# Performance work log

Measured on AMD Instinct MI355X. Metric: run time of the kernel, lower is better.

Reference implementation:

```python
import jax, jax.numpy as jnp
import numpy as np

N = 150000   # nonempty octree nodes at this depth
CIN = 256
CB = 64      # bottleneck channels = out_channels / bottleneck
COUT = 256
G = 32       # group-norm groups
K = 27       # 3x3x3 neighborhood
EPS = 1e-5


def group_norm(x, gamma, beta, groups=G):
    # x: [N, C]; octree GN treats the N nodes as the spatial extent of one instance
    n, c = x.shape
    xg = x.reshape(n, groups, c // groups)
    mu = xg.mean(axis=(0, 2), keepdims=True)
    var = xg.var(axis=(0, 2), keepdims=True)
    xg = (xg - mu) * jax.lax.rsqrt(var + EPS)
    return xg.reshape(n, c) * gamma + beta


def setup_inputs() -> dict:
    key = jax.random.key(0)
    ks = jax.random.split(key, 5)
    return {
        "data": jax.random.normal(ks[0], (N, CIN), jnp.float32),
        "neigh": jax.random.randint(ks[1], (N, K), 0, N, jnp.int32),
        "w1a": jax.random.normal(ks[2], (CIN, CB), jnp.float32) * 0.05,
        "g1a": jnp.ones((CB,), jnp.float32),
        "b1a": jnp.zeros((CB,), jnp.float32),
        "w3": jax.random.normal(ks[3], (K, CB, CB), jnp.float32) * 0.05,
        "g3": jnp.ones((CB,), jnp.float32),
        "b3": jnp.zeros((CB,), jnp.float32),
        "w1b": jax.random.normal(ks[4], (CB, COUT), jnp.float32) * 0.05,
        "g1b": jnp.ones((COUT,), jnp.float32),
        "b1b": jnp.zeros((COUT,), jnp.float32),
    }


def reference(data, neigh, w1a, g1a, b1a, w3, g3, b3, w1b, g1b, b1b):
    # conv1x1a + GN + ReLU
    x = jax.nn.relu(group_norm(data @ w1a, g1a, b1a))
    # octree 3x3x3 sparse conv: gather 27 neighbors, GEMM against [27,CB,CB] kernel
    gathered = x[neigh]                      # [N, 27, CB]
    y = jnp.einsum('nkc,kcd->nd', gathered, w3)
    y = jax.nn.relu(group_norm(y, g3, b3))
    # conv1x1b + GN
    z = group_norm(y @ w1b, g1b, b1b)
    # residual add (in_channels == out_channels -> identity skip) + ReLU
    return jax.nn.relu(z + data)
```

## Files before the change

kernel.cpp:

```cpp
#include <hip/hip_runtime.h>
#include <math.h>

#define CIN 256
#define CB 64
#define COUT 256
#define KNB 27
#define EPS 1e-5f

typedef unsigned short u16;
typedef __attribute__((ext_vector_type(8))) short short8;
typedef __attribute__((ext_vector_type(4))) float f32x4;

typedef const __attribute__((address_space(1))) unsigned int* gas_u32p;
typedef __attribute__((address_space(3))) unsigned int* las_u32p;
#define GLL(g, p) __builtin_amdgcn_global_load_lds((gas_u32p)(const void*)(g), \
        (las_u32p)(void*)(p), 16, 0, 0)

__device__ inline short f2bf(float f) {
    union { float f; unsigned u; } v; v.f = f;
    unsigned r = v.u + 0x7fff + ((v.u >> 16) & 1);
    return (short)(r >> 16);
}
__device__ inline float bf2f(short s) {
    union { unsigned u; float f; } v; v.u = ((unsigned)(u16)s) << 16;
    return v.f;
}
__device__ inline short8 pack8(float4 x0, float4 x1) {
    short8 r;
    r[0] = f2bf(x0.x); r[1] = f2bf(x0.y); r[2] = f2bf(x0.z); r[3] = f2bf(x0.w);
    r[4] = f2bf(x1.x); r[5] = f2bf(x1.y); r[6] = f2bf(x1.z); r[7] = f2bf(x1.w);
    return r;
}

__global__ void k_prep(const float* __restrict__ w1a, const float* __restrict__ w3,
                       const float* __restrict__ w1b, u16* __restrict__ w1at,
                       u16* __restrict__ w3img, u16* __restrict__ w1bt)
{
    int i = blockIdx.x * 256 + threadIdx.x;
    if (i < 16384) {
        int k = i >> 6, d = i & 63;
        w1at[d * 256 + k] = (u16)f2bf(w1a[i]);
    } else if (i < 126976) {
        int j = i - 16384;
        int k = j >> 12, c = (j >> 6) & 63, d = j & 63;
        w3img[(size_t)k * 4096 + d * 64 + (c ^ ((d & 7) << 3))] = (u16)f2bf(w3[j]);
    } else if (i < 143360) {
        int j = i - 126976;
        int c = j >> 8, d = j & 255;
        w1bt[d * 64 + c] = (u16)f2bf(w1b[j]);
    }
}

__global__ __launch_bounds__(256) void k_gemm1(const float* __restrict__ data,
        const u16* __restrict__ w1at, u16* __restrict__ t1,
        float* __restrict__ stats, int n)
{
    __shared__ float s_sum[32], s_sq[32];
    const int tid = threadIdx.x;
    if (tid < 32) { s_sum[tid] = 0.f; s_sq[tid] = 0.f; }
    __syncthreads();
    const int l = tid & 63, wv = tid >> 6;
    const int ll = l & 15, lh = l >> 4;
    const int rowbase = blockIdx.x * 256 + wv * 64;

    f32x4 acc[4][4] = {};
#pragma unroll
    for (int kc = 0; kc < 8; ++kc) {
        short8 b[4];
#pragma unroll
        for (int f = 0; f < 4; ++f)
            b[f] = *(const short8*)(w1at + (size_t)(f * 16 + ll) * 256 + kc * 32 + lh * 8);
#pragma unroll
        for (int rt = 0; rt < 4; ++rt) {
            int row = rowbase + rt * 16 + ll;
            int rowc = (row < n) ? row : 0;
            const float* ar = data + (size_t)rowc * CIN + kc * 32 + lh * 8;
            short8 a = pack8(*(const float4*)ar, *(const float4*)(ar + 4));
#pragma unroll
            for (int f = 0; f < 4; ++f)
                acc[rt][f] = __builtin_amdgcn_mfma_f32_16x16x32_bf16(a, b[f], acc[rt][f], 0, 0, 0);
        }
    }
    float gs[4] = {0.f, 0.f, 0.f, 0.f}, gq[4] = {0.f, 0.f, 0.f, 0.f};
#pragma unroll
    for (int rt = 0; rt < 4; ++rt) {
#pragma unroll
        for (int f = 0; f < 4; ++f) {
#pragma unroll
            for (int r = 0; r < 4; ++r) {
                int rr = rowbase + rt * 16 + lh * 4 + r;
                if (rr < n) {
                    float v = acc[rt][f][r];
                    t1[(size_t)rr * CB + f * 16 + ll] = (u16)f2bf(v);
                    gs[f] += v; gq[f] += v * v;
                }
            }
        }
    }
#pragma unroll
    for (int f = 0; f < 4; ++f) {
        float s = gs[f], q = gq[f];
        s += __shfl_xor(s, 1); s += __shfl_xor(s, 16); s += __shfl_xor(s, 32);
        q += __shfl_xor(q, 1); q += __shfl_xor(q, 16); q += __shfl_xor(q, 32);
        if ((l & 0x31) == 0) {
            atomicAdd(&s_sum[f * 8 + (ll >> 1)], s);
            atomicAdd(&s_sq [f * 8 + (ll >> 1)], q);
        }
    }
    __syncthreads();
    if (tid < 32) {
        atomicAdd(&stats[tid], s_sum[tid]);
        atomicAdd(&stats[32 + tid], s_sq[tid]);
    }
}

__global__ void k_apply64(u16* __restrict__ buf, const float* __restrict__ st,
        const float* __restrict__ gamma, const float* __restrict__ beta, int n)
{
    const float cnt = (float)n * 2.0f;
    const int total = n * 8;
    for (int i = blockIdx.x * blockDim.x + threadIdx.x; i < total;
         i += gridDim.x * blockDim.x) {
        int c0 = (i & 7) * 8;
        short8 v = ((short8*)buf)[i];
#pragma unroll
        for (int j = 0; j < 8; ++j) {
            int c = c0 + j, g = c >> 1;
            float mu = st[g] / cnt;
            float var = st[32 + g] / cnt - mu * mu;
            float inv = rsqrtf(var + EPS);
            float x = bf2f(v[j]);
            x = fmaxf((x - mu) * inv * gamma[c] + beta[c], 0.f);
            v[j] = f2bf(x);
        }
        ((short8*)buf)[i] = v;
    }
}

__global__ __launch_bounds__(256) void k_conv(const u16* __restrict__ xb,
        const int* __restrict__ neigh, const u16* __restrict__ w3img,
        u16* __restrict__ y, float* __restrict__ stats, int n)
{
    __shared__ u16 s_w3[2][4096];
    __shared__ float s_sum[32], s_sq[32];
    const int tid = threadIdx.x;
    if (tid < 32) { s_sum[tid] = 0.f; s_sq[tid] = 0.f; }
    const int row0 = blockIdx.x * 128;
    const int l = tid & 63, wv = tid >> 6;
    const int ll = l & 15, lh = l >> 4;
    const int r0 = row0 + wv * 32 + ll;
    const int r1 = r0 + 16;
    const int r0c = (r0 < n) ? r0 : 0;
    const int r1c = (r1 < n) ? r1 : 0;
    const int* __restrict__ nrow0 = neigh + (size_t)r0c * KNB;
    const int* __restrict__ nrow1 = neigh + (size_t)r1c * KNB;

    u16* ld0 = &s_w3[0][0] + wv * 1024 + l * 8;
    u16* ld1 = &s_w3[1][0] + wv * 1024 + l * 8;
    const u16* gw = w3img + wv * 1024 + l * 8;

    GLL(gw, ld0);
    GLL(gw + 512, ld0 + 512);
    int ia = nrow0[0], ib = nrow1[0];
    {
        const u16* xa = xb + (size_t)ia * CB + lh * 8;
        const u16* xc = xb + (size_t)ib * CB + lh * 8;
        ia = nrow0[1]; ib = nrow1[1];
        __builtin_amdgcn_sched_barrier(0);
    }
    short8 a0c, a1c, a2c, a3c;
    {
        const u16* xa = xb + (size_t)nrow0[0] * CB + lh * 8;
        const u16* xc = xb + (size_t)nrow1[0] * CB + lh * 8;
        a0c = *(const short8*)xa; a1c = *(const short8*)(xa + 32);
        a2c = *(const short8*)xc; a3c = *(const short8*)(xc + 32);
    }
    __syncthreads();

    f32x4 acc[2][4] = {};
    for (int k = 0; k < KNB; ++k) {
        const int cur = k & 1;
        short8 a0n, a1n, a2n, a3n;
        if (k + 1 < KNB) {
            const u16* gsrc = w3img + (size_t)(k + 1) * 4096 + wv * 1024 + l * 8;
            u16* ldst = cur ? ld0 : ld1;
            GLL(gsrc, ldst);
            GLL(gsrc + 512, ldst + 512);
            int i2 = nrow0[k + 1], i3 = nrow1[k + 1];
            const u16* xa = xb + (size_t)i2 * CB + lh * 8;
            const u16* xc = xb + (size_t)i3 * CB + lh * 8;
            a0n = *(const short8*)xa; a1n = *(const short8*)(xa + 32);
            a2n = *(const short8*)xc; a3n = *(const short8*)(xc + 32);
        }
        __builtin_amdgcn_sched_barrier(0);
#pragma unroll
        for (int f = 0; f < 4; ++f) {
            int d = f * 16 + ll;
            int swz = (d & 7) << 4;
            short8 b0 = *(const short8*)((const char*)&s_w3[cur][0] + d * 128 + ((lh * 16) ^ swz));
            short8 b1 = *(const short8*)((const char*)&s_w3[cur][0] + d * 128 + ((64 + lh * 16) ^ swz));
            acc[0][f] = __builtin_amdgcn_mfma_f32_16x16x32_bf16(a0c, b0, acc[0][f], 0, 0, 0);
            acc[0][f] = __builtin_amdgcn_mfma_f32_16x16x32_bf16(a1c, b1, acc[0][f], 0, 0, 0);
            acc[1][f] = __builtin_amdgcn_mfma_f32_16x16x32_bf16(a2c, b0, acc[1][f], 0, 0, 0);
            acc[1][f] = __builtin_amdgcn_mfma_f32_16x16x32_bf16(a3c, b1, acc[1][f], 0, 0, 0);
        }
        if (k + 1 < KNB) { a0c = a0n; a1c = a1n; a2c = a2n; a3c = a3n; }
        __syncthreads();
    }
    float gs[4] = {0.f, 0.f, 0.f, 0.f}, gq[4] = {0.f, 0.f, 0.f, 0.f};
#pragma unroll
    for (int rt = 0; rt < 2; ++rt) {
#pragma unroll
        for (int f = 0; f < 4; ++f) {
#pragma unroll
            for (int r = 0; r < 4; ++r) {
                int rr = row0 + wv * 32 + rt * 16 + lh * 4 + r;
                if (rr < n) {
                    float v = acc[rt][f][r];
                    y[(size_t)rr * CB + f * 16 + ll] = (u16)f2bf(v);
                    gs[f] += v; gq[f] += v * v;
                }
            }
        }
    }
#pragma unroll
    for (int f = 0; f < 4; ++f) {
        float s = gs[f], q = gq[f];
        s += __shfl_xor(s, 1); s += __shfl_xor(s, 16); s += __shfl_xor(s, 32);
        q += __shfl_xor(q, 1); q += __shfl_xor(q, 16); q += __shfl_xor(q, 32);
        if ((l & 0x31) == 0) {
            atomicAdd(&s_sum[f * 8 + (ll >> 1)], s);
            atomicAdd(&s_sq [f * 8 + (ll >> 1)], q);
        }
    }
    __syncthreads();
    if (tid < 32) {
        atomicAdd(&stats[64 + tid], s_sum[tid]);
        atomicAdd(&stats[96 + tid], s_sq[tid]);
    }
}

__global__ __launch_bounds__(256) void k_gemm2(const u16* __restrict__ y2,
        const u16* __restrict__ w1bt, float* __restrict__ z, u16* __restrict__ zb,
        float* __restrict__ stats, const float* __restrict__ g3,
        const float* __restrict__ b3, int n)
{
    __shared__ float s_sum[8], s_sq[8];
    const int tid = threadIdx.x;
    if (tid < 8) { s_sum[tid] = 0.f; s_sq[tid] = 0.f; }
    __syncthreads();
    const int l = tid & 63, wv = tid >> 6;
    const int ll = l & 15, lh = l >> 4;
    const int rowbase = blockIdx.x * 256 + wv * 64;
    const int cb = blockIdx.y;

    const float* st2 = stats + 64;
    const float cnt2 = (float)n * 2.0f;
    float sc[16], sh[16];
#pragma unroll
    for (int j = 0; j < 16; ++j) {
        int c = (j < 8) ? (lh * 8 + j) : (32 + lh * 8 + (j - 8));
        int g = c >> 1;
        float mu = st2[g] / cnt2;
        float var = st2[32 + g] / cnt2 - mu * mu;
        float inv = rsqrtf(var + EPS);
        float gm = g3[c];
        sc[j] = inv * gm;
        sh[j] = b3[c] - mu * inv * gm;
    }

    short8 b0[4], b1[4];
#pragma unroll
    for (int f = 0; f < 4; ++f) {
        const u16* br = w1bt + (size_t)(cb * 64 + f * 16 + ll) * CB + lh * 8;
        b0[f] = *(const short8*)(br);
        b1[f] = *(const short8*)(br + 32);
    }
    f32x4 acc[4][4] = {};
#pragma unroll
    for (int rt = 0; rt < 4; ++rt) {
        int row = rowbase + rt * 16 + ll;
        int rowc = (row < n) ? row : 0;
        const u16* ar = y2 + (size_t)rowc * CB + lh * 8;
        short8 r0 = *(const short8*)(ar);
        short8 r1 = *(const short8*)(ar + 32);
        short8 a0, a1;
#pragma unroll
        for (int j = 0; j < 8; ++j) {
            a0[j] = f2bf(fmaxf(bf2f(r0[j]) * sc[j] + sh[j], 0.f));
            a1[j] = f2bf(fmaxf(bf2f(r1[j]) * sc[8 + j] + sh[8 + j], 0.f));
        }
#pragma unroll
        for (int f = 0; f < 4; ++f) {
            acc[rt][f] = __builtin_amdgcn_mfma_f32_16x16x32_bf16(a0, b0[f], acc[rt][f], 0, 0, 0);
            acc[rt][f] = __builtin_amdgcn_mfma_f32_16x16x32_bf16(a1, b1[f], acc[rt][f], 0, 0, 0);
        }
    }
    float gs[4] = {0.f, 0.f, 0.f, 0.f}, gq[4] = {0.f, 0.f, 0.f, 0.f};
#pragma unroll
    for (int rt = 0; rt < 4; ++rt) {
#pragma unroll
        for (int f = 0; f < 4; ++f) {
#pragma unroll
            for (int r = 0; r < 4; ++r) {
                int rr = rowbase + rt * 16 + lh * 4 + r;
                if (rr < n) {
                    float v = acc[rt][f][r];
                    size_t off = (size_t)rr * COUT + cb * 64 + f * 16 + ll;
                    if (zb) zb[off] = (u16)f2bf(v); else z[off] = v;
                    gs[f] += v; gq[f] += v * v;
                }
            }
        }
    }
#pragma unroll
    for (int f = 0; f < 4; ++f) {
        float s = gs[f], q = gq[f];
        s += __shfl_xor(s, 1); s += __shfl_xor(s, 2); s += __shfl_xor(s, 4);
        s += __shfl_xor(s, 16); s += __shfl_xor(s, 32);
        q += __shfl_xor(q, 1); q += __shfl_xor(q, 2); q += __shfl_xor(q, 4);
        q += __shfl_xor(q, 16); q += __shfl_xor(q, 32);
        if ((l & 0x37) == 0) {
            atomicAdd(&s_sum[f * 2 + (ll >> 3)], s);
            atomicAdd(&s_sq [f * 2 + (ll >> 3)], q);
        }
    }
    __syncthreads();
    if (tid < 8) {
        atomicAdd(&stats[128 + cb * 8 + tid], s_sum[tid]);
        atomicAdd(&stats[160 + cb * 8 + tid], s_sq[tid]);
    }
}

__global__ void k_final_bf(float* __restrict__ out, const u16* __restrict__ zb,
        const float* __restrict__ data, const float* __restrict__ st,
        const float* __restrict__ gamma, const float* __restrict__ beta, int n)
{
    const float cnt = (float)n * 8.0f;
    const int total = n * 32;
    for (int i = blockIdx.x * blockDim.x + threadIdx.x; i < total;
         i += gridDim.x * blockDim.x) {
        int c0 = (i & 31) * 8;
        int g = c0 >> 3;
        float mu = st[g] / cnt;
        float var = st[32 + g] / cnt - mu * mu;
        float inv = rsqrtf(var + EPS);
        short8 zv = ((const short8*)zb)[i];
        float dd[8], oo[8];
        *(float4*)dd = *(const float4*)(data + (size_t)i * 8);
        *(float4*)(dd + 4) = *(const float4*)(data + (size_t)i * 8 + 4);
#pragma unroll
        for (int j = 0; j < 8; ++j)
            oo[j] = fmaxf((bf2f(zv[j]) - mu) * inv * gamma[c0 + j] + beta[c0 + j] + dd[j], 0.f);
        *(float4*)(out + (size_t)i * 8) = *(float4*)oo;
        *(float4*)(out + (size_t)i * 8 + 4) = *(float4*)(oo + 4);
    }
}

__global__ void k_final(float* __restrict__ zo, const float* __restrict__ data,
        const float* __restrict__ st, const float* __restrict__ gamma,
        const float* __restrict__ beta, int n)
{
    const float cnt = (float)n * 8.0f;
    const int total = n * (COUT / 4);
    for (int i = blockIdx.x * blockDim.x + threadIdx.x; i < total;
         i += gridDim.x * blockDim.x) {
        int c4 = (i & (COUT / 4 - 1)) * 4;
        int g = c4 >> 3;
        float mu = st[g] / cnt;
        float var = st[32 + g] / cnt - mu * mu;
        float inv = rsqrtf(var + EPS);
        float4 zv = *(float4*)(zo + (size_t)i * 4);
        float4 dv = *(const float4*)(data + (size_t)i * 4);
        zv.x = fmaxf((zv.x - mu) * inv * gamma[c4 + 0] + beta[c4 + 0] + dv.x, 0.f);
        zv.y = fmaxf((zv.y - mu) * inv * gamma[c4 + 1] + beta[c4 + 1] + dv.y, 0.f);
        zv.z = fmaxf((zv.z - mu) * inv * gamma[c4 + 2] + beta[c4 + 2] + dv.z, 0.f);
        zv.w = fmaxf((zv.w - mu) * inv * gamma[c4 + 3] + beta[c4 + 3] + dv.w, 0.f);
        *(float4*)(zo + (size_t)i * 4) = zv;
    }
}

extern "C" void kernel_launch(void* const* d_in, const int* in_sizes, int n_in,
                              void* d_out, int out_size, void* d_ws, size_t ws_size,
                              hipStream_t stream)
{
    const float* data = (const float*)d_in[0];
    const int*   neigh = (const int*)d_in[1];
    const float* w1a = (const float*)d_in[2];
    const float* g1a = (const float*)d_in[3];
    const float* b1a = (const float*)d_in[4];
    const float* w3  = (const float*)d_in[5];
    const float* g3  = (const float*)d_in[6];
    const float* b3  = (const float*)d_in[7];
    const float* w1b = (const float*)d_in[8];
    const float* g1b = (const float*)d_in[9];
    const float* b1b = (const float*)d_in[10];
    float* out = (float*)d_out;
    float* ws  = (float*)d_ws;

    const int n = in_sizes[0] / CIN;

    float* stats = ws;
    u16* w1at  = (u16*)(ws + 256);
    u16* w3img = w1at + 16384;
    u16* w1bt  = w3img + 110592;
    u16* t1    = w1bt + 16384;
    u16* ybuf  = t1 + (size_t)n * CB;
    u16* zb    = nullptr;
    {
        size_t need = 1024 + 286720 + (size_t)n * CB * 4 + (size_t)n * COUT * 2;
        if (ws_size >= need) zb = ybuf + (size_t)n * CB;
    }

    hipMemsetAsync(stats, 0, 192 * sizeof(float), stream);

    const int nb128 = (n + 127) / 128;
    const int nb256 = (n + 255) / 256;
    k_prep<<<560, 256, 0, stream>>>(w1a, w3, w1b, w1at, w3img, w1bt);
    k_gemm1<<<nb256, 256, 0, stream>>>(data, w1at, t1, stats, n);
    k_apply64<<<2048, 256, 0, stream>>>(t1, stats, g1a, b1a, n);
    k_conv<<<nb128, 256, 0, stream>>>(t1, neigh, w3img, ybuf, stats, n);
    k_gemm2<<<dim3(nb256, 4), 256, 0, stream>>>(ybuf, w1bt, out, zb, stats, g3, b3, n);
    if (zb)
        k_final_bf<<<2048, 256, 0, stream>>>(out, zb, data, stats + 128, g1b, b1b, n);
    else
        k_final<<<2048, 256, 0, stream>>>(out, data, stats + 128, g1b, b1b, n);
}
```

Measured before the change: 292.6 us.

## Load conv weights directly to registers and deepen gather prefetch pipeline

The sparse conv kernel stops staging per-offset weight slices through LDS with global_load_lds and block barriers. Each lane now loads its B fragments straight from a plain transposed weight image in global memory (L1/L2 resident), double-buffered in registers. Neighbor-feature gathers are prefetched two offsets ahead with a triple-buffered register ring, and neighbor indices three ahead. The fully unrolled loop removes all __syncthreads, at the cost of redundant weight loads per wave and higher register pressure that may lower occupancy.

```diff
diff --git a/kernel.cpp b/kernel.cpp
--- a/kernel.cpp
+++ b/kernel.cpp
@@ -11,11 +11,6 @@
 typedef __attribute__((ext_vector_type(8))) short short8;
 typedef __attribute__((ext_vector_type(4))) float f32x4;
 
-typedef const __attribute__((address_space(1))) unsigned int* gas_u32p;
-typedef __attribute__((address_space(3))) unsigned int* las_u32p;
-#define GLL(g, p) __builtin_amdgcn_global_load_lds((gas_u32p)(const void*)(g), \
-        (las_u32p)(void*)(p), 16, 0, 0)
-
 __device__ inline short f2bf(float f) {
     union { float f; unsigned u; } v; v.f = f;
     unsigned r = v.u + 0x7fff + ((v.u >> 16) & 1);
@@ -34,7 +29,7 @@
 
 __global__ void k_prep(const float* __restrict__ w1a, const float* __restrict__ w3,
                        const float* __restrict__ w1b, u16* __restrict__ w1at,
-                       u16* __restrict__ w3img, u16* __restrict__ w1bt)
+                       u16* __restrict__ w3t, u16* __restrict__ w1bt)
 {
     int i = blockIdx.x * 256 + threadIdx.x;
     if (i < 16384) {
@@ -43,7 +38,7 @@
     } else if (i < 126976) {
         int j = i - 16384;
         int k = j >> 12, c = (j >> 6) & 63, d = j & 63;
-        w3img[(size_t)k * 4096 + d * 64 + (c ^ ((d & 7) << 3))] = (u16)f2bf(w3[j]);
+        w3t[(size_t)k * 4096 + d * 64 + c] = (u16)f2bf(w3[j]);
     } else if (i < 143360) {
         int j = i - 126976;
         int c = j >> 8, d = j & 255;
@@ -138,10 +133,9 @@
 }
 
 __global__ __launch_bounds__(256) void k_conv(const u16* __restrict__ xb,
-        const int* __restrict__ neigh, const u16* __restrict__ w3img,
+        const int* __restrict__ neigh, const u16* __restrict__ w3t,
         u16* __restrict__ y, float* __restrict__ stats, int n)
 {
-    __shared__ u16 s_w3[2][4096];
     __shared__ float s_sum[32], s_sq[32];
     const int tid = threadIdx.x;
     if (tid < 32) { s_sum[tid] = 0.f; s_sq[tid] = 0.f; }
@@ -154,59 +148,64 @@
     const int r1c = (r1 < n) ? r1 : 0;
     const int* __restrict__ nrow0 = neigh + (size_t)r0c * KNB;
     const int* __restrict__ nrow1 = neigh + (size_t)r1c * KNB;
-
-    u16* ld0 = &s_w3[0][0] + wv * 1024 + l * 8;
-    u16* ld1 = &s_w3[1][0] + wv * 1024 + l * 8;
-    const u16* gw = w3img + wv * 1024 + l * 8;
-
-    GLL(gw, ld0);
-    GLL(gw + 512, ld0 + 512);
-    int ia = nrow0[0], ib = nrow1[0];
+    const u16* __restrict__ bbase = w3t + ll * 64 + lh * 8;
+
+    short8 A[3][4];
+    short8 Bv[2][8];
+    int idxq[2][2];
+
     {
-        const u16* xa = xb + (size_t)ia * CB + lh * 8;
-        const u16* xc = xb + (size_t)ib * CB + lh * 8;
-        ia = nrow0[1]; ib = nrow1[1];
+        int i0 = nrow0[0], i1 = nrow1[0], i2 = nrow0[1], i3 = nrow1[1];
+        const u16* xa = xb + (size_t)i0 * CB + lh * 8;
+        const u16* xc = xb + (size_t)i1 * CB + lh * 8;
+        A[0][0] = *(const short8*)xa; A[0][1] = *(const short8*)(xa + 32);
+        A[0][2] = *(const short8*)xc; A[0][3] = *(const short8*)(xc + 32);
+        const u16* xe = xb + (size_t)i2 * CB + lh * 8;
+        const u16* xg = xb + (size_t)i3 * CB + lh * 8;
+        A[1][0] = *(const short8*)xe; A[1][1] = *(const short8*)(xe + 32);
+        A[1][2] = *(const short8*)xg; A[1][3] = *(const short8*)(xg + 32);
+#pragma unroll
+        for (int f = 0; f < 4; ++f) {
+            Bv[0][f]     = *(const short8*)(bbase + f * 1024);
+            Bv[0][4 + f] = *(const short8*)(bbase + f * 1024 + 32);
+        }
+        idxq[0][0] = nrow0[2]; idxq[0][1] = nrow1[2];
+    }
+
+    f32x4 acc[2][4] = {};
+#pragma unroll
+    for (int k = 0; k < KNB; ++k) {
+        if (k + 1 < KNB) {
+            const u16* bp = bbase + (size_t)(k + 1) * 4096;
+#pragma unroll
+            for (int f = 0; f < 4; ++f) {
+                Bv[(k + 1) & 1][f]     = *(const short8*)(bp + f * 1024);
+                Bv[(k + 1) & 1][4 + f] = *(const short8*)(bp + f * 1024 + 32);
+            }
+        }
+        if (k + 2 < KNB) {
+            int i0 = idxq[k & 1][0], i1 = idxq[k & 1][1];
+            const u16* xa = xb + (size_t)i0 * CB + lh * 8;
+            const u16* xc = xb + (size_t)i1 * CB + lh * 8;
+            A[(k + 2) % 3][0] = *(const short8*)xa;
+            A[(k + 2) % 3][1] = *(const short8*)(xa + 32);
+            A[(k + 2) % 3][2] = *(const short8*)xc;
+            A[(k + 2) % 3][3] = *(const short8*)(xc + 32);
+        }
+        if (k + 3 < KNB) {
+            idxq[(k + 1) & 1][0] = nrow0[k + 3];
+            idxq[(k + 1) & 1][1] = nrow1[k + 3];
+        }
         __builtin_amdgcn_sched_barrier(0);
-    }
-    short8 a0c, a1c, a2c, a3c;
-    {
-        const u16* xa = xb + (size_t)nrow0[0] * CB + lh * 8;
-        const u16* xc = xb + (size_t)nrow1[0] * CB + lh * 8;
-        a0c = *(const short8*)xa; a1c = *(const short8*)(xa + 32);
-        a2c = *(const short8*)xc; a3c = *(const short8*)(xc + 32);
-    }
-    __syncthreads();
-
-    f32x4 acc[2][4] = {};
-    for (int k = 0; k < KNB; ++k) {
-        const int cur = k & 1;
-        short8 a0n, a1n, a2n, a3n;
-        if (k + 1 < KNB) {
-            const u16* gsrc = w3img + (size_t)(k + 1) * 4096 + wv * 1024 + l * 8;
-            u16* ldst = cur ? ld0 : ld1;
-            GLL(gsrc, ldst);
-            GLL(gsrc + 512, ldst + 512);
-            int i2 = nrow0[k + 1], i3 = nrow1[k + 1];
-            const u16* xa = xb + (size_t)i2 * CB + lh * 8;
-            const u16* xc = xb + (size_t)i3 * CB + lh * 8;
-            a0n = *(const short8*)xa; a1n = *(const short8*)(xa + 32);
-            a2n = *(const short8*)xc; a3n = *(const short8*)(xc + 32);
-        }
-        __builtin_amdgcn_sched_barrier(0);
-#pragma unroll
-        for (int f = 0; f < 4; ++f) {
-            int d = f * 16 + ll;
-            int swz = (d & 7) << 4;
-            short8 b0 = *(const short8*)((const char*)&s_w3[cur][0] + d * 128 + ((lh * 16) ^ swz));
-            short8 b1 = *(const short8*)((const char*)&s_w3[cur][0] + d * 128 + ((64 + lh * 16) ^ swz));
-            acc[0][f] = __builtin_amdgcn_mfma_f32_16x16x32_bf16(a0c, b0, acc[0][f], 0, 0, 0);
-            acc[0][f] = __builtin_amdgcn_mfma_f32_16x16x32_bf16(a1c, b1, acc[0][f], 0, 0, 0);
-            acc[1][f] = __builtin_amdgcn_mfma_f32_16x16x32_bf16(a2c, b0, acc[1][f], 0, 0, 0);
-            acc[1][f] = __builtin_amdgcn_mfma_f32_16x16x32_bf16(a3c, b1, acc[1][f], 0, 0, 0);
-        }
-        if (k + 1 < KNB) { a0c = a0n; a1c = a1n; a2c = a2n; a3c = a3n; }
-        __syncthreads();
-    }
+#pragma unroll
+        for (int f = 0; f < 4; ++f) {
+            acc[0][f] = __builtin_amdgcn_mfma_f32_16x16x32_bf16(A[k % 3][0], Bv[k & 1][f],     acc[0][f], 0, 0, 0);
+            acc[0][f] = __builtin_amdgcn_mfma_f32_16x16x32_bf16(A[k % 3][1], Bv[k & 1][4 + f], acc[0][f], 0, 0, 0);
+            acc[1][f] = __builtin_amdgcn_mfma_f32_16x16x32_bf16(A[k % 3][2], Bv[k & 1][f],     acc[1][f], 0, 0, 0);
+            acc[1][f] = __builtin_amdgcn_mfma_f32_16x16x32_bf16(A[k % 3][3], Bv[k & 1][4 + f], acc[1][f], 0, 0, 0);
+        }
+    }
+
     float gs[4] = {0.f, 0.f, 0.f, 0.f}, gq[4] = {0.f, 0.f, 0.f, 0.f};
 #pragma unroll
     for (int rt = 0; rt < 2; ++rt) {
@@ -401,12 +400,12 @@
     const int n = in_sizes[0] / CIN;
 
     float* stats = ws;
-    u16* w1at  = (u16*)(ws + 256);
-    u16* w3img = w1at + 16384;
-    u16* w1bt  = w3img + 110592;
-    u16* t1    = w1bt + 16384;
-    u16* ybuf  = t1 + (size_t)n * CB;
-    u16* zb    = nullptr;
+    u16* w1at = (u16*)(ws + 256);
+    u16* w3t  = w1at + 16384;
+    u16* w1bt = w3t + 110592;
+    u16* t1   = w1bt + 16384;
+    u16* ybuf = t1 + (size_t)n * CB;
+    u16* zb   = nullptr;
     {
         size_t need = 1024 + 286720 + (size_t)n * CB * 4 + (size_t)n * COUT * 2;
         if (ws_size >= need) zb = ybuf + (size_t)n * CB;
@@ -416,10 +415,10 @@
 
     const int nb128 = (n + 127) / 128;
     const int nb256 = (n + 255) / 256;
-    k_prep<<<560, 256, 0, stream>>>(w1a, w3, w1b, w1at, w3img, w1bt);
+    k_prep<<<560, 256, 0, stream>>>(w1a, w3, w1b, w1at, w3t, w1bt);
     k_gemm1<<<nb256, 256, 0, stream>>>(data, w1at, t1, stats, n);
     k_apply64<<<2048, 256, 0, stream>>>(t1, stats, g1a, b1a, n);
-    k_conv<<<nb128, 256, 0, stream>>>(t1, neigh, w3img, ybuf, stats, n);
+    k_conv<<<nb128, 256, 0, stream>>>(t1, neigh, w3t, ybuf, stats, n);
     k_gemm2<<<dim3(nb256, 4), 256, 0, stream>>>(ybuf, w1bt, out, zb, stats, g3, b3, n);
     if (zb)
         k_final_bf<<<2048, 256, 0, stream>>>(out, zb, data, stats + 128, g1b, b1b, n);
```

New measurement: 380.7 us. 30.1% more time.

## Prefetch neighbor indices two steps ahead and use partial waitcnt barriers in sparse conv loop

Applied to the files above, without the earlier changes.

Loads the neighbor indices one iteration earlier than before, so the row gathers for step k+1 no longer wait on an index load issued in the same iteration. Replaces __syncthreads with explicit s_waitcnt vmcnt(N) plus s_barrier, so the next tile's global loads can stay in flight across the barrier. Also fully unrolls the 27-step loop. The hand-counted vmcnt values rely on the compiler's instruction order; if it reorders, reads of LDS or registers could race.

```diff
diff --git a/kernel.cpp b/kernel.cpp
--- a/kernel.cpp
+++ b/kernel.cpp
@@ -161,37 +161,36 @@
 
     GLL(gw, ld0);
     GLL(gw + 512, ld0 + 512);
-    int ia = nrow0[0], ib = nrow1[0];
-    {
-        const u16* xa = xb + (size_t)ia * CB + lh * 8;
-        const u16* xc = xb + (size_t)ib * CB + lh * 8;
-        ia = nrow0[1]; ib = nrow1[1];
-        __builtin_amdgcn_sched_barrier(0);
-    }
+    int ia0 = nrow0[0], ib0 = nrow1[0];
+    int ian = nrow0[1], ibn = nrow1[1];
     short8 a0c, a1c, a2c, a3c;
     {
-        const u16* xa = xb + (size_t)nrow0[0] * CB + lh * 8;
-        const u16* xc = xb + (size_t)nrow1[0] * CB + lh * 8;
+        const u16* xa = xb + (size_t)ia0 * CB + lh * 8;
+        const u16* xc = xb + (size_t)ib0 * CB + lh * 8;
         a0c = *(const short8*)xa; a1c = *(const short8*)(xa + 32);
         a2c = *(const short8*)xc; a3c = *(const short8*)(xc + 32);
     }
-    __syncthreads();
+    asm volatile("s_waitcnt vmcnt(8) lgkmcnt(0)" ::: "memory");
+    __builtin_amdgcn_s_barrier();
+    __builtin_amdgcn_sched_barrier(0);
 
     f32x4 acc[2][4] = {};
+#pragma unroll
     for (int k = 0; k < KNB; ++k) {
         const int cur = k & 1;
         short8 a0n, a1n, a2n, a3n;
+        int iaf = 0, ibf = 0;
         if (k + 1 < KNB) {
             const u16* gsrc = w3img + (size_t)(k + 1) * 4096 + wv * 1024 + l * 8;
             u16* ldst = cur ? ld0 : ld1;
             GLL(gsrc, ldst);
             GLL(gsrc + 512, ldst + 512);
-            int i2 = nrow0[k + 1], i3 = nrow1[k + 1];
-            const u16* xa = xb + (size_t)i2 * CB + lh * 8;
-            const u16* xc = xb + (size_t)i3 * CB + lh * 8;
+            const u16* xa = xb + (size_t)ian * CB + lh * 8;
+            const u16* xc = xb + (size_t)ibn * CB + lh * 8;
             a0n = *(const short8*)xa; a1n = *(const short8*)(xa + 32);
             a2n = *(const short8*)xc; a3n = *(const short8*)(xc + 32);
         }
+        if (k + 2 < KNB) { iaf = nrow0[k + 2]; ibf = nrow1[k + 2]; }
         __builtin_amdgcn_sched_barrier(0);
 #pragma unroll
         for (int f = 0; f < 4; ++f) {
@@ -204,9 +203,18 @@
             acc[1][f] = __builtin_amdgcn_mfma_f32_16x16x32_bf16(a2c, b0, acc[1][f], 0, 0, 0);
             acc[1][f] = __builtin_amdgcn_mfma_f32_16x16x32_bf16(a3c, b1, acc[1][f], 0, 0, 0);
         }
-        if (k + 1 < KNB) { a0c = a0n; a1c = a1n; a2c = a2n; a3c = a3n; }
-        __syncthreads();
-    }
+        if (k + 1 < KNB) {
+            a0c = a0n; a1c = a1n; a2c = a2n; a3c = a3n;
+            ian = iaf; ibn = ibf;
+            if (k + 2 < KNB)
+                asm volatile("s_waitcnt vmcnt(6) lgkmcnt(0)" ::: "memory");
+            else
+                asm volatile("s_waitcnt vmcnt(4) lgkmcnt(0)" ::: "memory");
+            __builtin_amdgcn_s_barrier();
+            __builtin_amdgcn_sched_barrier(0);
+        }
+    }
+
     float gs[4] = {0.f, 0.f, 0.f, 0.f}, gq[4] = {0.f, 0.f, 0.f, 0.f};
 #pragma unroll
     for (int rt = 0; rt < 2; ++rt) {
```

Result: no change. 290.9 us (-0.6%).

## Stage three neighbor weight slices per barrier with deeper gather prefetch in sparse conv

Applied to the files above, without the earlier changes.

The 3x3x3 conv kernel now loads three neighbor weight matrices (24 KB) into each LDS double buffer instead of one, which cuts block barriers from 27 to 9. The neighbor-row gathers are prefetched two steps ahead through a 3-slot register ring, with index loads four steps ahead. Manual vmcnt waits replace __syncthreads. This aims to hide gather latency and reduce synchronisation, at the cost of more LDS (about 48 KB per block), which may lower occupancy, and fragile hand-counted waitcnt values.

```diff
diff --git a/kernel.cpp b/kernel.cpp
--- a/kernel.cpp
+++ b/kernel.cpp
@@ -141,7 +141,7 @@
         const int* __restrict__ neigh, const u16* __restrict__ w3img,
         u16* __restrict__ y, float* __restrict__ stats, int n)
 {
-    __shared__ u16 s_w3[2][4096];
+    __shared__ u16 s_w3[2][12288];
     __shared__ float s_sum[32], s_sq[32];
     const int tid = threadIdx.x;
     if (tid < 32) { s_sum[tid] = 0.f; s_sq[tid] = 0.f; }
@@ -150,63 +150,90 @@
     const int ll = l & 15, lh = l >> 4;
     const int r0 = row0 + wv * 32 + ll;
     const int r1 = r0 + 16;
-    const int r0c = (r0 < n) ? r0 : 0;
-    const int r1c = (r1 < n) ? r1 : 0;
-    const int* __restrict__ nrow0 = neigh + (size_t)r0c * KNB;
-    const int* __restrict__ nrow1 = neigh + (size_t)r1c * KNB;
-
-    u16* ld0 = &s_w3[0][0] + wv * 1024 + l * 8;
-    u16* ld1 = &s_w3[1][0] + wv * 1024 + l * 8;
-    const u16* gw = w3img + wv * 1024 + l * 8;
-
-    GLL(gw, ld0);
-    GLL(gw + 512, ld0 + 512);
-    int ia = nrow0[0], ib = nrow1[0];
+    const int* __restrict__ nrow0 = neigh + (size_t)((r0 < n) ? r0 : 0) * KNB;
+    const int* __restrict__ nrow1 = neigh + (size_t)((r1 < n) ? r1 : 0) * KNB;
+    const int so = wv * 3072 + l * 8;
+
+    short8 A[3][4];
+    int ixa[3], ixb[3];
+
+    ixa[0] = nrow0[0]; ixb[0] = nrow1[0];
+    ixa[1] = nrow0[1]; ixb[1] = nrow1[1];
+    __builtin_amdgcn_sched_barrier(0);
+#pragma unroll
+    for (int j = 0; j < 6; ++j)
+        GLL(w3img + so + j * 512, &s_w3[0][0] + so + j * 512);
+    __builtin_amdgcn_sched_barrier(0);
     {
-        const u16* xa = xb + (size_t)ia * CB + lh * 8;
-        const u16* xc = xb + (size_t)ib * CB + lh * 8;
-        ia = nrow0[1]; ib = nrow1[1];
+        const u16* xa = xb + (size_t)ixa[0] * CB + lh * 8;
+        const u16* xc = xb + (size_t)ixb[0] * CB + lh * 8;
+        A[0][0] = *(const short8*)xa; A[0][1] = *(const short8*)(xa + 32);
+        A[0][2] = *(const short8*)xc; A[0][3] = *(const short8*)(xc + 32);
+    }
+    {
+        const u16* xa = xb + (size_t)ixa[1] * CB + lh * 8;
+        const u16* xc = xb + (size_t)ixb[1] * CB + lh * 8;
+        A[1][0] = *(const short8*)xa; A[1][1] = *(const short8*)(xa + 32);
+        A[1][2] = *(const short8*)xc; A[1][3] = *(const short8*)(xc + 32);
+    }
+    ixa[2] = nrow0[2]; ixb[2] = nrow1[2];
+    ixa[0] = nrow0[3]; ixb[0] = nrow1[3];
+    asm volatile("s_waitcnt vmcnt(12) lgkmcnt(0)" ::: "memory");
+    __builtin_amdgcn_s_barrier();
+    __builtin_amdgcn_sched_barrier(0);
+
+    f32x4 acc[2][4] = {};
+#pragma unroll
+    for (int c = 0; c < 9; ++c) {
+        const int buf = c & 1;
+        if (c < 8) {
+            const u16* gsrc = w3img + (size_t)(c + 1) * 12288 + so;
+            u16* ldst = &s_w3[buf ^ 1][0] + so;
+#pragma unroll
+            for (int j = 0; j < 6; ++j)
+                GLL(gsrc + j * 512, ldst + j * 512);
+        }
         __builtin_amdgcn_sched_barrier(0);
-    }
-    short8 a0c, a1c, a2c, a3c;
-    {
-        const u16* xa = xb + (size_t)nrow0[0] * CB + lh * 8;
-        const u16* xc = xb + (size_t)nrow1[0] * CB + lh * 8;
-        a0c = *(const short8*)xa; a1c = *(const short8*)(xa + 32);
-        a2c = *(const short8*)xc; a3c = *(const short8*)(xc + 32);
-    }
-    __syncthreads();
-
-    f32x4 acc[2][4] = {};
-    for (int k = 0; k < KNB; ++k) {
-        const int cur = k & 1;
-        short8 a0n, a1n, a2n, a3n;
-        if (k + 1 < KNB) {
-            const u16* gsrc = w3img + (size_t)(k + 1) * 4096 + wv * 1024 + l * 8;
-            u16* ldst = cur ? ld0 : ld1;
-            GLL(gsrc, ldst);
-            GLL(gsrc + 512, ldst + 512);
-            int i2 = nrow0[k + 1], i3 = nrow1[k + 1];
-            const u16* xa = xb + (size_t)i2 * CB + lh * 8;
-            const u16* xc = xb + (size_t)i3 * CB + lh * 8;
-            a0n = *(const short8*)xa; a1n = *(const short8*)(xa + 32);
-            a2n = *(const short8*)xc; a3n = *(const short8*)(xc + 32);
-        }
-        __builtin_amdgcn_sched_barrier(0);
-#pragma unroll
-        for (int f = 0; f < 4; ++f) {
-            int d = f * 16 + ll;
-            int swz = (d & 7) << 4;
-            short8 b0 = *(const short8*)((const char*)&s_w3[cur][0] + d * 128 + ((lh * 16) ^ swz));
-            short8 b1 = *(const short8*)((const char*)&s_w3[cur][0] + d * 128 + ((64 + lh * 16) ^ swz));
-            acc[0][f] = __builtin_amdgcn_mfma_f32_16x16x32_bf16(a0c, b0, acc[0][f], 0, 0, 0);
-            acc[0][f] = __builtin_amdgcn_mfma_f32_16x16x32_bf16(a1c, b1, acc[0][f], 0, 0, 0);
-            acc[1][f] = __builtin_amdgcn_mfma_f32_16x16x32_bf16(a2c, b0, acc[1][f], 0, 0, 0);
-            acc[1][f] = __builtin_amdgcn_mfma_f32_16x16x32_bf16(a3c, b1, acc[1][f], 0, 0, 0);
-        }
-        if (k + 1 < KNB) { a0c = a0n; a1c = a1n; a2c = a2n; a3c = a3n; }
-        __syncthreads();
-    }
+#pragma unroll
+        for (int s = 0; s < 3; ++s) {
+            const int k = c * 3 + s;
+            if (k + 4 <= 26) {
+                ixa[(k + 4) % 3] = nrow0[k + 4];
+                ixb[(k + 4) % 3] = nrow1[k + 4];
+            }
+            __builtin_amdgcn_sched_barrier(0);
+            if (k + 2 <= 26) {
+                const u16* xa = xb + (size_t)ixa[(k + 2) % 3] * CB + lh * 8;
+                const u16* xc = xb + (size_t)ixb[(k + 2) % 3] * CB + lh * 8;
+                A[(k + 2) % 3][0] = *(const short8*)xa;
+                A[(k + 2) % 3][1] = *(const short8*)(xa + 32);
+                A[(k + 2) % 3][2] = *(const short8*)xc;
+                A[(k + 2) % 3][3] = *(const short8*)(xc + 32);
+            }
+            __builtin_amdgcn_sched_barrier(0);
+            const char* bpage = (const char*)&s_w3[buf][0] + s * 8192;
+#pragma unroll
+            for (int f = 0; f < 4; ++f) {
+                int d = f * 16 + ll;
+                int swz = (d & 7) << 4;
+                short8 b0 = *(const short8*)(bpage + d * 128 + ((lh * 16) ^ swz));
+                short8 b1 = *(const short8*)(bpage + d * 128 + ((64 + lh * 16) ^ swz));
+                acc[0][f] = __builtin_amdgcn_mfma_f32_16x16x32_bf16(A[k % 3][0], b0, acc[0][f], 0, 0, 0);
+                acc[0][f] = __builtin_amdgcn_mfma_f32_16x16x32_bf16(A[k % 3][1], b1, acc[0][f], 0, 0, 0);
+                acc[1][f] = __builtin_amdgcn_mfma_f32_16x16x32_bf16(A[k % 3][2], b0, acc[1][f], 0, 0, 0);
+                acc[1][f] = __builtin_amdgcn_mfma_f32_16x16x32_bf16(A[k % 3][3], b1, acc[1][f], 0, 0, 0);
+            }
+        }
+        if (c < 7)
+            asm volatile("s_waitcnt vmcnt(12) lgkmcnt(0)" ::: "memory");
+        else if (c == 7)
+            asm volatile("s_waitcnt vmcnt(10) lgkmcnt(0)" ::: "memory");
+        if (c < 8) {
+            __builtin_amdgcn_s_barrier();
+            __builtin_amdgcn_sched_barrier(0);
+        }
+    }
+
     float gs[4] = {0.f, 0.f, 0.f, 0.f}, gq[4] = {0.f, 0.f, 0.f, 0.f};
 #pragma unroll
     for (int rt = 0; rt < 2; ++rt) {
```

Result: faster. 283.9 us, median of 2 (-3.0%).
